# Optimization experiments

Measured on AMD Instinct MI355X. Metric: run time of the kernel, lower is better.

The kernel has to match this reference:

```python
import jax, jax.numpy as jnp
import numpy as np

DIM, INNER, NH = 256, 64, 8
HD = INNER // NH  # 8
B, H, W = 2, 48, 48
EPS = 1e-6


def _ln2d(x, w, b):
    # channel-first LayerNorm over dim=1, biased variance (matches LayerNorm2d)
    u = x.mean(axis=1, keepdims=True)
    s = ((x - u) ** 2).mean(axis=1, keepdims=True)
    xn = (x - u) / jnp.sqrt(s + EPS)
    return w[None, :, None, None] * xn + b[None, :, None, None]


def _conv1x1(x, w, b):
    return jnp.einsum('oc,bchw->bohw', w, x) + b[None, :, None, None]


def _attn(q, k, v):
    # q,k,v: [B, INNER, H, W] -> global attention over HW tokens per head
    Bq, C, Hh, Ww = q.shape
    split = lambda t: t.reshape(Bq, NH, HD, Hh * Ww)
    q, k, v = split(q), split(k), split(v)
    scale = HD ** -0.5
    attn = jnp.einsum('bhdn,bhdm->bhnm', q, k) * scale  # [B,nh,HW,HW]
    attn = jax.nn.softmax(attn, axis=-1)
    out = jnp.einsum('bhnm,bhdm->bhdn', attn, v)
    return out.reshape(Bq, C, Hh, Ww)


def setup_inputs() -> dict:
    key = jax.random.key(0)
    ks = jax.random.split(key, 12)
    w = lambda k, o, i: jax.random.normal(k, (o, i), dtype=jnp.float32) * 0.02
    d = {
        'f_rgb': jax.random.normal(ks[0], (B, DIM, H, W), dtype=jnp.float32),
        'f_ir': jax.random.normal(ks[1], (B, DIM, H, W), dtype=jnp.float32),
        'nr_w': jnp.ones(DIM), 'nr_b': jnp.zeros(DIM),
        'ni_w': jnp.ones(DIM), 'ni_b': jnp.zeros(DIM),
        'qr_w': w(ks[2], INNER, DIM), 'qr_b': jnp.zeros(INNER),
        'kvi_w': w(ks[3], 2 * INNER, DIM), 'kvi_b': jnp.zeros(2 * INNER),
        'qi_w': w(ks[4], INNER, DIM), 'qi_b': jnp.zeros(INNER),
        'kvr_w': w(ks[5], 2 * INNER, DIM), 'kvr_b': jnp.zeros(2 * INNER),
        'pr_w': w(ks[6], DIM, INNER), 'pr_b': jnp.zeros(DIM),
        'pr_lnw': jnp.ones(DIM), 'pr_lnb': jnp.zeros(DIM),
        'pi_w': w(ks[7], DIM, INNER), 'pi_b': jnp.zeros(DIM),
        'pi_lnw': jnp.ones(DIM), 'pi_lnb': jnp.zeros(DIM),
        'gr_w': w(ks[8], DIM, 2 * DIM), 'gr_b': jnp.zeros(DIM),
        'gi_w': w(ks[9], DIM, 2 * DIM), 'gi_b': jnp.zeros(DIM),
    }
    return d


def reference(f_rgb, f_ir, nr_w, nr_b, ni_w, ni_b, qr_w, qr_b, kvi_w, kvi_b,
              qi_w, qi_b, kvr_w, kvr_b, pr_w, pr_b, pr_lnw, pr_lnb,
              pi_w, pi_b, pi_lnw, pi_lnb, gr_w, gr_b, gi_w, gi_b):
    n_rgb = _ln2d(f_rgb, nr_w, nr_b)
    n_ir = _ln2d(f_ir, ni_w, ni_b)

    # RGB queries attend to IR keys/values
    q_r = _conv1x1(n_rgb, qr_w, qr_b)
    kv_i = _conv1x1(n_ir, kvi_w, kvi_b)
    k_i, v_i = kv_i[:, :INNER], kv_i[:, INNER:]
    rgb_cross = _attn(q_r, k_i, v_i)
    rgb_cross = _ln2d(_conv1x1(rgb_cross, pr_w, pr_b), pr_lnw, pr_lnb)
    gate_r = jax.nn.sigmoid(_conv1x1(jnp.concatenate([f_rgb, rgb_cross], axis=1), gr_w, gr_b))
    f_rgb_out = f_rgb + gate_r * rgb_cross

    # IR queries attend to RGB keys/values
    q_i = _conv1x1(n_ir, qi_w, qi_b)
    kv_r = _conv1x1(n_rgb, kvr_w, kvr_b)
    k_r, v_r = kv_r[:, :INNER], kv_r[:, INNER:]
    ir_cross = _attn(q_i, k_r, v_r)
    ir_cross = _ln2d(_conv1x1(ir_cross, pi_w, pi_b), pi_lnw, pi_lnb)
    gate_i = jax.nn.sigmoid(_conv1x1(jnp.concatenate([f_ir, ir_cross], axis=1), gi_w, gi_b))
    f_ir_out = f_ir + gate_i * ir_cross

    return (f_rgb_out, f_ir_out)
```

## Files before the change

kernel.cpp:

```cpp
#include <hip/hip_runtime.h>

static constexpr int kDim   = 256;
static constexpr int kInner = 64;
static constexpr int kNH    = 8;
static constexpr int kB     = 2;
static constexpr int kP     = 2304;
static constexpr float kScale = 0.35355339059327373f;
static constexpr float kEps   = 1e-6f;

typedef __fp16   fp16x2 __attribute__((ext_vector_type(2)));
typedef _Float16 half4f __attribute__((ext_vector_type(4)));
typedef _Float16 half8  __attribute__((ext_vector_type(8)));
typedef float    f32x4  __attribute__((ext_vector_type(4)));

static constexpr size_t oXq  = 0;
static constexpr size_t oQ16 = 2359296;
static constexpr size_t oK16 = 2949120;
static constexpr size_t oV16 = 3538944;
static constexpr size_t oA16 = 4128768;
static constexpr size_t oC16 = 4718592;
static constexpr size_t oW16 = 7077888;
static constexpr size_t kInpStride = 294912;

__global__ __launch_bounds__(256) void prep(
    const float* __restrict__ x0, const float* __restrict__ w0,
    const float* __restrict__ b0, const float* __restrict__ x1,
    const float* __restrict__ w1, const float* __restrict__ b1,
    _Float16* __restrict__ Xq,
    const float* __restrict__ qr_w, const float* __restrict__ kvr_w,
    const float* __restrict__ qi_w, const float* __restrict__ kvi_w,
    const float* __restrict__ pr_w, const float* __restrict__ pi_w,
    const float* __restrict__ gr_w, const float* __restrict__ gi_w,
    _Float16* __restrict__ w16)
{
    if (blockIdx.x >= 576) {
        const int flat = blockIdx.x - 576;
        const int y = flat >> 6, x = flat & 63;
        const float* src; _Float16* dst; int n;
        _Float16* Aq = w16;
        _Float16* Ap = w16 + 98304;
        _Float16* Ag = w16 + 131072;
        switch (y) {
            case 0: src = qr_w;  dst = Aq;          n = 16384;  break;
            case 1: src = kvr_w; dst = Aq + 16384;  n = 32768;  break;
            case 2: src = qi_w;  dst = Aq + 49152;  n = 16384;  break;
            case 3: src = kvi_w; dst = Aq + 65536;  n = 32768;  break;
            case 4: src = pr_w;  dst = Ap;          n = 16384;  break;
            case 5: src = pi_w;  dst = Ap + 16384;  n = 16384;  break;
            case 6: src = gr_w;  dst = Ag;          n = 131072; break;
            default:src = gi_w;  dst = Ag + 131072; n = 131072; break;
        }
        for (int i = x * 256 + threadIdx.x; i < n; i += 64 * 256)
            dst[i] = (_Float16)src[i];
        return;
    }
    __shared__ float sb[16][16];
    __shared__ float ssb[16][16];
    const int fid = blockIdx.x;
    const int xcd = fid & 7, q = fid >> 3;
    const int inp = (xcd >> 2) & 1, bb = (xcd >> 1) & 1, half = xcd & 1;
    const float* x = inp ? x1 : x0;
    const float* w = inp ? w1 : w0;
    const float* b = inp ? b1 : b0;
    const int pos = threadIdx.x & 15;
    const int grp = threadIdx.x >> 4;
    const int p   = half * 1152 + q * 16 + pos;
    const size_t base = (size_t)bb * kDim * kP + p;
    const int c0 = grp * 16;

    float v[16];
    float s = 0.f, ss = 0.f;
    #pragma unroll
    for (int j = 0; j < 16; ++j) {
        v[j] = x[base + (size_t)(c0 + j) * kP];
        s += v[j]; ss += v[j] * v[j];
    }
    sb[grp][pos] = s; ssb[grp][pos] = ss;
    __syncthreads();
    float st = 0.f, sst = 0.f;
    #pragma unroll
    for (int g = 0; g < 16; ++g) { st += sb[g][pos]; sst += ssb[g][pos]; }
    const float mean = st * (1.f / kDim);
    const float rstd = rsqrtf(sst * (1.f / kDim) - mean * mean + kEps);
    half8 h0, h1;
    #pragma unroll
    for (int j = 0; j < 8; ++j) {
        h0[j] = (_Float16)((v[j]     - mean) * rstd * w[c0 + j]     + b[c0 + j]);
        h1[j] = (_Float16)((v[j + 8] - mean) * rstd * w[c0 + j + 8] + b[c0 + j + 8]);
    }
    _Float16* dst = Xq + ((size_t)(inp * 2 + bb) * kP + p) * 256 + c0;
    *(half8*)dst       = h0;
    *(half8*)(dst + 8) = h1;
}

__global__ __launch_bounds__(256) void ln_post(
    const _Float16* __restrict__ c16,
    const float* __restrict__ w0, const float* __restrict__ b0,
    const float* __restrict__ w1, const float* __restrict__ b1,
    const float* __restrict__ f0, const float* __restrict__ f1,
    _Float16* __restrict__ Xg)
{
    __shared__ float sb[16][16];
    __shared__ float ssb[16][16];
    const int fid = blockIdx.x;
    const int xcd = fid & 7, q = fid >> 3;
    const int s = (xcd >> 2) & 1, bb = (xcd >> 1) & 1, half = xcd & 1;
    const float* w = s ? w1 : w0;
    const float* b = s ? b1 : b0;
    const float* F = s ? f1 : f0;
    const int pos = threadIdx.x & 15;
    const int grp = threadIdx.x >> 4;
    const int p   = half * 1152 + q * 16 + pos;
    const int c0  = grp * 16;
    const size_t combo = s * 2 + bb;

    const _Float16* cp = c16 + (combo * kP + p) * 256 + c0;
    const half8 g0 = *(const half8*)cp;
    const half8 g1 = *(const half8*)(cp + 8);
    float v[16];
    float sm = 0.f, ssq = 0.f;
    #pragma unroll
    for (int j = 0; j < 8; ++j) {
        v[j] = (float)g0[j]; v[j + 8] = (float)g1[j];
    }
    #pragma unroll
    for (int j = 0; j < 16; ++j) { sm += v[j]; ssq += v[j] * v[j]; }
    sb[grp][pos] = sm; ssb[grp][pos] = ssq;
    __syncthreads();
    float st = 0.f, sst = 0.f;
    #pragma unroll
    for (int g = 0; g < 16; ++g) { st += sb[g][pos]; sst += ssb[g][pos]; }
    const float mean = st * (1.f / kDim);
    const float rstd = rsqrtf(sst * (1.f / kDim) - mean * mean + kEps);

    _Float16* xrow = Xg + (combo * kP + p) * 512;
    half8 o0, o1;
    #pragma unroll
    for (int j = 0; j < 8; ++j) {
        o0[j] = (_Float16)((v[j]     - mean) * rstd * w[c0 + j]     + b[c0 + j]);
        o1[j] = (_Float16)((v[j + 8] - mean) * rstd * w[c0 + j + 8] + b[c0 + j + 8]);
    }
    *(half8*)(xrow + 256 + c0)     = o0;
    *(half8*)(xrow + 256 + c0 + 8) = o1;
    const size_t fbase = (size_t)bb * kDim * kP + p;
    half8 r0, r1;
    #pragma unroll
    for (int j = 0; j < 8; ++j) {
        r0[j] = (_Float16)F[fbase + (size_t)(c0 + j) * kP];
        r1[j] = (_Float16)F[fbase + (size_t)(c0 + j + 8) * kP];
    }
    *(half8*)(xrow + c0)     = r0;
    *(half8*)(xrow + c0 + 8) = r1;
}

template <int M, int K, int EPI>
__global__ __launch_bounds__(256) void gemm_f16(
    const _Float16* __restrict__ A,
    const _Float16* __restrict__ B,
    const float* __restrict__ b0, const float* __restrict__ b1,
    const float* __restrict__ b2, const float* __restrict__ b3,
    _Float16* __restrict__ o16a, _Float16* __restrict__ o16b, _Float16* __restrict__ o16c,
    const float* __restrict__ f0, const float* __restrict__ f1,
    float* __restrict__ outp)
{
    constexpr int MT64 = M / 64;
    const int fid = blockIdx.x;
    const int xcd = fid & 7, q = fid >> 3;
    const int s = (xcd >> 2) & 1, bb = (xcd >> 1) & 1, half = xcd & 1;
    const int ot64 = (q % MT64) * 64;
    const int pt   = q / MT64;
    const int wv = threadIdx.x >> 6, lane = threadIdx.x & 63;
    const int r16 = lane & 15, g = lane >> 4;
    const int ot = ot64 + wv * 16;
    const int p0 = half * 1152 + pt * 64;
    const int combo = s * 2 + bb;

    const _Float16* Ar = A + ((size_t)s * M + ot + r16) * K + 8 * g;
    const _Float16* Br = B + ((size_t)combo * kP + p0 + r16) * K + 8 * g;
    f32x4 acc0[4], acc1[4];
    #pragma unroll
    for (int ps = 0; ps < 4; ++ps) {
        acc0[ps] = (f32x4){0.f, 0.f, 0.f, 0.f};
        acc1[ps] = (f32x4){0.f, 0.f, 0.f, 0.f};
    }
    #pragma unroll 4
    for (int c0 = 0; c0 < K; c0 += 32) {
        const half8 a8 = *(const half8*)(Ar + c0);
        half8 b8[4];
        #pragma unroll
        for (int ps = 0; ps < 4; ++ps)
            b8[ps] = *(const half8*)(Br + (size_t)(16 * ps) * K + c0);
        const half4f al = {a8[0], a8[1], a8[2], a8[3]};
        const half4f ah = {a8[4], a8[5], a8[6], a8[7]};
        #pragma unroll
        for (int ps = 0; ps < 4; ++ps) {
            const half4f bl = {b8[ps][0], b8[ps][1], b8[ps][2], b8[ps][3]};
            const half4f bh = {b8[ps][4], b8[ps][5], b8[ps][6], b8[ps][7]};
            acc0[ps] = __builtin_amdgcn_mfma_f32_16x16x16f16(al, bl, acc0[ps], 0, 0, 0);
            acc1[ps] = __builtin_amdgcn_mfma_f32_16x16x16f16(ah, bh, acc1[ps], 0, 0, 0);
        }
    }
    const int obase = ot + 4 * g;

    #pragma unroll
    for (int ps = 0; ps < 4; ++ps) {
        float acc[4];
        #pragma unroll
        for (int i = 0; i < 4; ++i) acc[i] = acc0[ps][i] + acc1[ps][i];
        const int p = p0 + 16 * ps + r16;

        if constexpr (EPI == 0) {
            const int dlo = 4 * (g & 1);
            if (ot < 64) {
                const float* qb = s ? b1 : b0;
                const float4 bv = *(const float4*)(qb + obase);
                const int h = (ot >> 3) + (g >> 1);
                half4f o = { (_Float16)((acc[0] + bv.x) * kScale), (_Float16)((acc[1] + bv.y) * kScale),
                             (_Float16)((acc[2] + bv.z) * kScale), (_Float16)((acc[3] + bv.w) * kScale) };
                *(half4f*)(o16a + (((size_t)combo * 8 + h) * kP + p) * 8 + dlo) = o;
            } else if (ot < 128) {
                const float* kb = s ? b3 : b2;
                const float4 bv = *(const float4*)(kb + obase - 64);
                const int h = ((ot - 64) >> 3) + (g >> 1);
                half4f o = { (_Float16)(acc[0] + bv.x), (_Float16)(acc[1] + bv.y),
                             (_Float16)(acc[2] + bv.z), (_Float16)(acc[3] + bv.w) };
                *(half4f*)(o16b + (((size_t)combo * 8 + h) * kP + p) * 8 + dlo) = o;
            } else {
                const float* kb = s ? b3 : b2;
                const float4 bv = *(const float4*)(kb + obase - 64);
                const int h = ((ot - 128) >> 3) + (g >> 1);
                const float* bvp = (const float*)&bv;
                #pragma unroll
                for (int i = 0; i < 4; ++i)
                    o16c[(((size_t)combo * 8 + h) * 8 + dlo + i) * kP + p] = (_Float16)(acc[i] + bvp[i]);
            }
        } else if constexpr (EPI == 1) {
            const float* pb = s ? b1 : b0;
            const float4 bv = *(const float4*)(pb + obase);
            half4f o = { (_Float16)(acc[0] + bv.x), (_Float16)(acc[1] + bv.y),
                         (_Float16)(acc[2] + bv.z), (_Float16)(acc[3] + bv.w) };
            *(half4f*)(o16a + ((size_t)combo * kP + p) * 256 + obase) = o;
        } else {
            const float* gb = s ? b1 : b0;
            const float4 bv = *(const float4*)(gb + obase);
            const float* bvp = (const float*)&bv;
            const half4f cx = *(const half4f*)(B + ((size_t)combo * kP + p) * 512 + 256 + obase);
            const float* F = s ? f1 : f0;
            #pragma unroll
            for (int i = 0; i < 4; ++i) {
                const int o = obase + i;
                const float gt = 1.f / (1.f + __expf(-(acc[i] + bvp[i])));
                const float fb = F[((size_t)bb * kDim + o) * kP + p];
                outp[((size_t)combo * kDim + o) * kP + p] = fb + gt * (float)cx[i];
            }
        }
    }
}

__global__ __launch_bounds__(256) void attn_mfma(
    const _Float16* __restrict__ q16, const _Float16* __restrict__ k16,
    const _Float16* __restrict__ vt16, _Float16* __restrict__ a16)
{
    __shared__ _Float16 Ksm[16 * 64 * 4];
    __shared__ _Float16 Vsm[16 * 64 * 4];
    const int st = blockIdx.z;
    const _Float16* Qg = q16  + (size_t)st * kInpStride;
    const _Float16* Kg = k16  + (size_t)(1 - st) * kInpStride;
    const _Float16* Vg = vt16 + (size_t)(1 - st) * kInpStride;
    const int bh = blockIdx.y;
    const int bb = bh >> 3, h = bh & 7;
    const int tid  = threadIdx.x;
    const int wv   = tid >> 6;
    const int lane = tid & 63;
    const int r16  = lane & 15;
    const int g    = lane >> 4;

    #pragma unroll
    for (int j = 0; j < 2; ++j) {
        const int s = tid + 256 * j;
        const int kt = s >> 5, m = s & 31;
        *(half4f*)(Ksm + (kt * 64 + 32 + m) * 4) = (half4f){0, 0, 0, 0};
        const int rv = 8 + (m & 7), gv = m >> 3;
        const half4f vv = (rv == 8)
            ? (half4f){(_Float16)1.f, (_Float16)1.f, (_Float16)1.f, (_Float16)1.f}
            : (half4f){0, 0, 0, 0};
        *(half4f*)(Vsm + (kt * 64 + gv * 16 + rv) * 4) = vv;
    }

    const int qg = blockIdx.x * 64 + wv * 16 + r16;
    half4f qf = (half4f){0, 0, 0, 0};
    if (g < 2) qf = *(const half4f*)(Qg + ((size_t)bh * kP + qg) * 8 + g * 4);

    f32x4 of = (f32x4){0.f, 0.f, 0.f, 0.f};

    for (int ch = 0; ch < 9; ++ch) {
        if (ch) __syncthreads();
        const int p0 = ch * 256;
        {
            const half8 k8 = *(const half8*)(Kg + ((size_t)bh * kP + p0 + tid) * 8);
            _Float16* base = Ksm + ((tid >> 4) * 64 + (tid & 15)) * 4;
            *(half4f*)base        = (half4f){k8[0], k8[1], k8[2], k8[3]};
            *(half4f*)(base + 64) = (half4f){k8[4], k8[5], k8[6], k8[7]};
        }
        {
            const int d = tid >> 5, c8 = (tid & 31) * 8;
            const half8 v8 = *(const half8*)(Vg + (size_t)(bh * 8 + d) * kP + p0 + c8);
            const int kt = c8 >> 4, gv = (c8 & 15) >> 2;
            _Float16* base = Vsm + (kt * 64 + gv * 16 + d) * 4;
            *(half4f*)base        = (half4f){v8[0], v8[1], v8[2], v8[3]};
            *(half4f*)(base + 64) = (half4f){v8[4], v8[5], v8[6], v8[7]};
        }
        __syncthreads();
        #pragma unroll
        for (int kt = 0; kt < 16; ++kt) {
            const half4f kf = *(const half4f*)(Ksm + kt * 256 + lane * 4);
            f32x4 sv = __builtin_amdgcn_mfma_f32_16x16x16f16(kf, qf, (f32x4){0.f,0.f,0.f,0.f}, 0, 0, 0);
            const float e0 = __expf(sv[0]), e1 = __expf(sv[1]);
            const float e2 = __expf(sv[2]), e3 = __expf(sv[3]);
            const fp16x2 lo = __builtin_amdgcn_cvt_pkrtz(e0, e1);
            const fp16x2 hi = __builtin_amdgcn_cvt_pkrtz(e2, e3);
            const half4f pf = { (_Float16)lo[0], (_Float16)lo[1],
                                (_Float16)hi[0], (_Float16)hi[1] };
            const half4f vf = *(const half4f*)(Vsm + kt * 256 + lane * 4);
            of = __builtin_amdgcn_mfma_f32_16x16x16f16(vf, pf, of, 0, 0, 0);
        }
    }
    const float rsv = __shfl(of[0], 32 + r16, 64);
    const float inv = 1.f / rsv;
    if (g < 2) {
        half4f o = { (_Float16)(of[0] * inv), (_Float16)(of[1] * inv),
                     (_Float16)(of[2] * inv), (_Float16)(of[3] * inv) };
        *(half4f*)(a16 + ((size_t)(st * 2 + bb) * kP + qg) * 64 + h * 8 + g * 4) = o;
    }
}

extern "C" void kernel_launch(void* const* d_in, const int* in_sizes, int n_in,
                              void* d_out, int out_size, void* d_ws, size_t ws_size,
                              hipStream_t stream)
{
    const float* f_rgb  = (const float*)d_in[0];
    const float* f_ir   = (const float*)d_in[1];
    const float* nr_w   = (const float*)d_in[2];
    const float* nr_b   = (const float*)d_in[3];
    const float* ni_w   = (const float*)d_in[4];
    const float* ni_b   = (const float*)d_in[5];
    const float* qr_w   = (const float*)d_in[6];
    const float* qr_b   = (const float*)d_in[7];
    const float* kvi_w  = (const float*)d_in[8];
    const float* kvi_b  = (const float*)d_in[9];
    const float* qi_w   = (const float*)d_in[10];
    const float* qi_b   = (const float*)d_in[11];
    const float* kvr_w  = (const float*)d_in[12];
    const float* kvr_b  = (const float*)d_in[13];
    const float* pr_w   = (const float*)d_in[14];
    const float* pr_b   = (const float*)d_in[15];
    const float* pr_lnw = (const float*)d_in[16];
    const float* pr_lnb = (const float*)d_in[17];
    const float* pi_w   = (const float*)d_in[18];
    const float* pi_b   = (const float*)d_in[19];
    const float* pi_lnw = (const float*)d_in[20];
    const float* pi_lnb = (const float*)d_in[21];
    const float* gr_w   = (const float*)d_in[22];
    const float* gr_b   = (const float*)d_in[23];
    const float* gi_w   = (const float*)d_in[24];
    const float* gi_b   = (const float*)d_in[25];

    _Float16* hb   = (_Float16*)d_ws;
    _Float16* Xq   = hb + oXq;
    _Float16* q16  = hb + oQ16;
    _Float16* k16  = hb + oK16;
    _Float16* vt16 = hb + oV16;
    _Float16* a16  = hb + oA16;
    _Float16* Xg   = hb;
    _Float16* c16  = hb + oC16;
    _Float16* W16  = hb + oW16;
    _Float16* Aq   = W16;
    _Float16* Ap   = W16 + 98304;
    _Float16* Ag   = W16 + 131072;

    float* outp = (float*)d_out;
    const dim3 blk(256);

    prep<<<dim3(1088), blk, 0, stream>>>(f_rgb, nr_w, nr_b, f_ir, ni_w, ni_b, Xq,
                                         qr_w, kvr_w, qi_w, kvi_w, pr_w, pi_w, gr_w, gi_w, W16);
    gemm_f16<192, 256, 0><<<dim3(432), blk, 0, stream>>>(
        Aq, Xq, qr_b, qi_b, kvr_b, kvi_b, q16, k16, vt16, nullptr, nullptr, nullptr);
    attn_mfma<<<dim3(36, 16, 2), blk, 0, stream>>>(q16, k16, vt16, a16);
    gemm_f16<256, 64, 1><<<dim3(576), blk, 0, stream>>>(
        Ap, a16, pr_b, pi_b, nullptr, nullptr, c16, nullptr, nullptr, nullptr, nullptr, nullptr);
    ln_post<<<dim3(576), blk, 0, stream>>>(c16, pr_lnw, pr_lnb, pi_lnw, pi_lnb,
                                           f_rgb, f_ir, Xg);
    gemm_f16<256, 512, 2><<<dim3(576), blk, 0, stream>>>(
        Ag, Xg, gr_b, gi_b, nullptr, nullptr, nullptr, nullptr, nullptr, f_rgb, f_ir, outp);
}
```

Before: 111.7 us.

## Prefetch next K/V chunk into registers and pad V shared-memory tiles

The attention kernel now issues the global loads for the next 256-key chunk of K and V into registers right after the barrier, so they overlap with the MFMA and exp work on the current chunk instead of stalling at the top of each iteration. The V shared-memory layout gets a stride of 66 instead of 64 per key tile, aimed at reducing LDS bank conflicts on the strided V stores. The cost is extra live registers and a slightly larger LDS footprint.

```diff
diff --git a/kernel.cpp b/kernel.cpp
--- a/kernel.cpp
+++ b/kernel.cpp
@@ -262,7 +262,7 @@
     const _Float16* __restrict__ vt16, _Float16* __restrict__ a16)
 {
     __shared__ _Float16 Ksm[16 * 64 * 4];
-    __shared__ _Float16 Vsm[16 * 64 * 4];
+    __shared__ _Float16 Vsm[16 * 66 * 4];
     const int st = blockIdx.z;
     const _Float16* Qg = q16  + (size_t)st * kInpStride;
     const _Float16* Kg = k16  + (size_t)(1 - st) * kInpStride;
@@ -284,36 +284,39 @@
         const half4f vv = (rv == 8)
             ? (half4f){(_Float16)1.f, (_Float16)1.f, (_Float16)1.f, (_Float16)1.f}
             : (half4f){0, 0, 0, 0};
-        *(half4f*)(Vsm + (kt * 64 + gv * 16 + rv) * 4) = vv;
+        *(half4f*)(Vsm + (kt * 66 + gv * 16 + rv) * 4) = vv;
     }
 
     const int qg = blockIdx.x * 64 + wv * 16 + r16;
     half4f qf = (half4f){0, 0, 0, 0};
     if (g < 2) qf = *(const half4f*)(Qg + ((size_t)bh * kP + qg) * 8 + g * 4);
 
+    const int vd = tid >> 5, vc8 = (tid & 31) * 8;
+    const int vkt = vc8 >> 4, vgv = (vc8 & 15) >> 2;
+    _Float16* kdst = Ksm + ((tid >> 4) * 64 + (tid & 15)) * 4;
+    _Float16* vdst = Vsm + (vkt * 66 + vgv * 16 + vd) * 4;
+    const _Float16* ksrc = Kg + ((size_t)bh * kP + tid) * 8;
+    const _Float16* vsrc = Vg + (size_t)(bh * 8 + vd) * kP + vc8;
+
+    half8 kreg = *(const half8*)ksrc;
+    half8 vreg = *(const half8*)vsrc;
+
     f32x4 of = (f32x4){0.f, 0.f, 0.f, 0.f};
 
     for (int ch = 0; ch < 9; ++ch) {
         if (ch) __syncthreads();
-        const int p0 = ch * 256;
-        {
-            const half8 k8 = *(const half8*)(Kg + ((size_t)bh * kP + p0 + tid) * 8);
-            _Float16* base = Ksm + ((tid >> 4) * 64 + (tid & 15)) * 4;
-            *(half4f*)base        = (half4f){k8[0], k8[1], k8[2], k8[3]};
-            *(half4f*)(base + 64) = (half4f){k8[4], k8[5], k8[6], k8[7]};
-        }
-        {
-            const int d = tid >> 5, c8 = (tid & 31) * 8;
-            const half8 v8 = *(const half8*)(Vg + (size_t)(bh * 8 + d) * kP + p0 + c8);
-            const int kt = c8 >> 4, gv = (c8 & 15) >> 2;
-            _Float16* base = Vsm + (kt * 64 + gv * 16 + d) * 4;
-            *(half4f*)base        = (half4f){v8[0], v8[1], v8[2], v8[3]};
-            *(half4f*)(base + 64) = (half4f){v8[4], v8[5], v8[6], v8[7]};
-        }
+        *(half4f*)kdst        = (half4f){kreg[0], kreg[1], kreg[2], kreg[3]};
+        *(half4f*)(kdst + 64) = (half4f){kreg[4], kreg[5], kreg[6], kreg[7]};
+        *(half4f*)vdst        = (half4f){vreg[0], vreg[1], vreg[2], vreg[3]};
+        *(half4f*)(vdst + 64) = (half4f){vreg[4], vreg[5], vreg[6], vreg[7]};
         __syncthreads();
+        if (ch < 8) {
+            kreg = *(const half8*)(ksrc + (size_t)(ch + 1) * 2048);
+            vreg = *(const half8*)(vsrc + (size_t)(ch + 1) * 256);
+        }
         #pragma unroll
         for (int kt = 0; kt < 16; ++kt) {
-            const half4f kf = *(const half4f*)(Ksm + kt * 256 + lane * 4);
+            const half4f kf = *(const half4f*)(Ksm + (kt * 64 + lane) * 4);
             f32x4 sv = __builtin_amdgcn_mfma_f32_16x16x16f16(kf, qf, (f32x4){0.f,0.f,0.f,0.f}, 0, 0, 0);
             const float e0 = __expf(sv[0]), e1 = __expf(sv[1]);
             const float e2 = __expf(sv[2]), e3 = __expf(sv[3]);
@@ -321,7 +324,7 @@
             const fp16x2 hi = __builtin_amdgcn_cvt_pkrtz(e2, e3);
             const half4f pf = { (_Float16)lo[0], (_Float16)lo[1],
                                 (_Float16)hi[0], (_Float16)hi[1] };
-            const half4f vf = *(const half4f*)(Vsm + kt * 256 + lane * 4);
+            const half4f vf = *(const half4f*)(Vsm + (kt * 66 + lane) * 4);
             of = __builtin_amdgcn_mfma_f32_16x16x16f16(vf, pf, of, 0, 0, 0);
         }
     }
```

Result: faster. 104.3 us (-6.7%).
